# Performance work log

Measured on AMD Instinct MI355X. Metric: run time of the kernel, lower is better.

## Reference

```python
import jax, jax.numpy as jnp
import numpy as np

B, S, DIM = 2, 2048, 2048
H = 16
Q_LORA, KV_LORA = 1536, 512
D_NOPE, D_ROPE, D_V = 128, 64, 128
D_QK = D_NOPE + D_ROPE  # 192
SCALE = D_QK ** -0.5
EPS = 1e-6
NEG = -1e30


def rmsnorm(x, w):
    return x * jax.lax.rsqrt(jnp.mean(x * x, axis=-1, keepdims=True) + EPS) * w


def apply_rope(x, cos, sin):
    # x: [..., S, ..., d] with adjacent-pair complex layout (torch view_as_complex)
    d2 = x.shape[-1] // 2
    xr = x.reshape(x.shape[:-1] + (d2, 2))
    x0, x1 = xr[..., 0], xr[..., 1]
    bshape = (1, cos.shape[0]) + (1,) * (x.ndim - 3) + (d2,)
    c, s = cos.reshape(bshape), sin.reshape(bshape)
    o0 = x0 * c - x1 * s
    o1 = x0 * s + x1 * c
    return jnp.stack([o0, o1], axis=-1).reshape(x.shape)


def setup_inputs() -> dict:
    key = jax.random.key(0)
    ks = jax.random.split(key, 6)
    inv_freq = 1.0 / (10000.0 ** (np.arange(0, D_ROPE, 2, dtype=np.float32) / D_ROPE))
    ang = np.arange(S, dtype=np.float32)[:, None] * inv_freq[None, :]  # [S, 32]
    return {
        "x": jax.random.normal(ks[0], (B, S, DIM), jnp.float32),
        "wq_a": jax.random.normal(ks[1], (Q_LORA, DIM), jnp.float32) * (DIM ** -0.5),
        "q_norm_w": jnp.ones((Q_LORA,), jnp.float32),
        "wq_b": jax.random.normal(ks[2], (H * D_QK, Q_LORA), jnp.float32) * (Q_LORA ** -0.5),
        "wkv_a": jax.random.normal(ks[3], (KV_LORA + D_ROPE, DIM), jnp.float32) * (DIM ** -0.5),
        "kv_norm_w": jnp.ones((KV_LORA,), jnp.float32),
        "wkv_b": jax.random.normal(ks[4], (H * (D_NOPE + D_V), KV_LORA), jnp.float32) * (KV_LORA ** -0.5),
        "wo": jax.random.normal(ks[5], (DIM, H * D_V), jnp.float32) * ((H * D_V) ** -0.5),
        "cos": jnp.asarray(np.cos(ang)),
        "sin": jnp.asarray(np.sin(ang)),
    }


def reference(x, wq_a, q_norm_w, wq_b, wkv_a, kv_norm_w, wkv_b, wo, cos, sin):
    b, s, _ = x.shape
    # low-rank query projection: wq_b(q_norm(wq_a(x)))
    q = jnp.einsum('bsd,rd->bsr', x, wq_a)
    q = rmsnorm(q, q_norm_w)
    q = jnp.einsum('bsr,or->bso', q, wq_b).reshape(b, s, H, D_QK)
    q_nope, q_pe = q[..., :D_NOPE], q[..., D_NOPE:]
    q_pe = apply_rope(q_pe, cos, sin)  # [b,s,h,64]

    # joint kv latent + rope key
    kv = jnp.einsum('bsd,od->bso', x, wkv_a)
    kv_c, k_pe = kv[..., :KV_LORA], kv[..., KV_LORA:]
    k_pe = apply_rope(k_pe, cos, sin)          # [b,t,64]
    kv_c = rmsnorm(kv_c, kv_norm_w)            # [b,t,c] latent kv cache

    # absorbed wkv_b: [H, d_nope+d_v, c]
    wkv_b_r = wkv_b.reshape(H, D_NOPE + D_V, KV_LORA)
    w_nope, w_v = wkv_b_r[:, :D_NOPE, :], wkv_b_r[:, D_NOPE:, :]

    q_abs = jnp.einsum('bshd,hdc->bshc', q_nope, w_nope)  # absorb K up-proj into q
    scores = (jnp.einsum('bshc,btc->bsht', q_abs, kv_c) +
              jnp.einsum('bshr,btr->bsht', q_pe, k_pe)) * SCALE

    causal = jnp.tril(jnp.ones((s, s), bool))  # [s, t]
    scores = jnp.where(causal[:, None, :], scores, NEG)

    attn = jax.nn.softmax(scores.astype(jnp.float32), axis=-1).astype(x.dtype)
    o = jnp.einsum('bsht,btc->bshc', attn, kv_c)       # attend in latent space
    o = jnp.einsum('bshc,hdc->bshd', o, w_v)           # absorb V up-proj
    out = jnp.einsum('bsf,of->bso', o.reshape(b, s, H * D_V), wo)
    return out
```

## Files before the change

kernel.cpp:

```cpp
#include <hip/hip_runtime.h>
#include <hip/hip_bf16.h>
#include <stdint.h>

#define B_    2
#define S_    2048
#define DIM_  2048
#define H_    16
#define QL_   1536
#define KVL_  512
#define DN_   128
#define DR_   64
#define DV_   128
#define DQK_  192
#define NKV_  576
#define NKVP_ 640
#define BS_   (B_*S_)
#define SCALE_ 0.07216878364870322f

typedef __hip_bfloat16 bf16;
typedef float f32x4 __attribute__((ext_vector_type(4)));
typedef short bf16x8 __attribute__((ext_vector_type(8)));

#define BMT 128
#define BNT 128
#define BKT 64

__device__ __forceinline__ void gload_lds16(const void* g, void* l) {
#if __has_builtin(__builtin_amdgcn_global_load_lds)
  __builtin_amdgcn_global_load_lds(
      (const __attribute__((address_space(1))) void*)g,
      (__attribute__((address_space(3))) void*)l, 16, 0, 0);
#else
  *(uint4*)l = *(const uint4*)g;
#endif
}

template <int K, int LDA, int LDB, int LDC, int FLAGS>
__global__ __launch_bounds__(512, 4) void gemm_t(
    const bf16* __restrict__ A, long saz,
    const bf16* __restrict__ Bm, long sbz,
    void* __restrict__ Cv, long scz)
{
  int z = blockIdx.z;
  A  += (long)z * saz;
  Bm += (long)z * sbz;
  long coff = (long)z * scz;

  int gx = gridDim.x;
  int lin = blockIdx.y * gx + blockIdx.x;
  int nwg = gx * gridDim.y;
  int wg = (lin & 7) * (nwg >> 3) + (lin >> 3);
  int ry = wg / gx, col0 = (wg % gx) * BNT;

  int tid = threadIdx.x, lane = tid & 63, wave = tid >> 6;
  int wm = (wave >> 2) * 64, wn = (wave & 3) * 32;
  int quad = lane >> 4, l16 = lane & 15;

  __shared__ __align__(16) bf16 Asm[BMT * BKT];
  __shared__ __align__(16) bf16 Bsm[BNT * BKT];

  const int npass = (FLAGS & 16) ? 2 : 1;
  const int nty = gridDim.y * ((FLAGS & 16) ? 2 : 1);

  for (int p = 0; p < npass; ++p) {
    int rt = (p == 0) ? ry : (nty - 1 - ry);
    int row0 = rt * BMT;

    if (FLAGS & 2) { if (col0 > row0 + (BMT - 1)) continue; }
    int kend = K;
    if (FLAGS & 4) { int lim = row0 + BMT; if (lim < kend) kend = lim; }

    f32x4 acc[4][2] = {};

    for (int k0 = 0; k0 < kend; k0 += BKT) {
      __syncthreads();
#pragma unroll
      for (int t = 0; t < 2; ++t) {
        int c = (wave * 2 + t) * 64 + lane;
        int m = c >> 3, jx = c & 7, j = jx ^ (m & 7);
        gload_lds16(A  + (long)((row0 + m) * LDA + k0 + j * 8), Asm + c * 8);
        gload_lds16(Bm + (long)((col0 + m) * LDB + k0 + j * 8), Bsm + c * 8);
      }
      __syncthreads();
#pragma unroll
      for (int kk = 0; kk < BKT; kk += 32) {
        int jl = (kk >> 3) + quad;
        bf16x8 af[4], bfv[2];
#pragma unroll
        for (int i = 0; i < 4; ++i) {
          int m = wm + i * 16 + l16;
          af[i]  = *(const bf16x8*)(Asm + m * 64 + ((jl ^ (m & 7)) * 8));
        }
#pragma unroll
        for (int jn = 0; jn < 2; ++jn) {
          int n = wn + jn * 16 + l16;
          bfv[jn] = *(const bf16x8*)(Bsm + n * 64 + ((jl ^ (n & 7)) * 8));
        }
#pragma unroll
        for (int i = 0; i < 4; ++i)
#pragma unroll
          for (int jn = 0; jn < 2; ++jn)
            acc[i][jn] = __builtin_amdgcn_mfma_f32_16x16x32_bf16(af[i], bfv[jn], acc[i][jn], 0, 0, 0);
      }
    }

    if (FLAGS & 1) {
      float* C = (float*)Cv + coff;
#pragma unroll
      for (int i = 0; i < 4; ++i)
#pragma unroll
        for (int jn = 0; jn < 2; ++jn)
#pragma unroll
          for (int r = 0; r < 4; ++r) {
            int rr = row0 + wm + i * 16 + quad * 4 + r;
            int cc = col0 + wn + jn * 16 + l16;
            C[(long)rr * LDC + cc] = acc[i][jn][r];
          }
    } else if (FLAGS & 8) {
      bf16* C = (bf16*)Cv + coff;
#pragma unroll
      for (int i = 0; i < 4; ++i)
#pragma unroll
        for (int jn = 0; jn < 2; ++jn)
#pragma unroll
          for (int r = 0; r < 4; ++r) {
            int rr = row0 + wm + i * 16 + quad * 4 + r;
            int cc = col0 + wn + jn * 16 + l16;
            C[(long)rr * LDC + cc] = __float2bfloat16(acc[i][jn][r] * SCALE_);
          }
    } else {
      bf16* C = (bf16*)Cv + coff;
#pragma unroll
      for (int i = 0; i < 4; ++i)
#pragma unroll
        for (int jn = 0; jn < 2; ++jn)
#pragma unroll
          for (int r = 0; r < 4; ++r) {
            int rr = row0 + wm + i * 16 + quad * 4 + r;
            int cc = col0 + wn + jn * 16 + l16;
            C[(long)rr * LDC + cc] = __float2bfloat16(acc[i][jn][r]);
          }
    }
  }
}

template <int K, int LDA, int LDB, int LDC, int FLAGS>
static inline void G(hipStream_t st, const bf16* A, long saz, const bf16* Bp, long sbz,
                     void* C, long scz, int M, int N, int Z) {
  int gy = M / BMT;
  if (FLAGS & 16) gy >>= 1;
  dim3 g(N / BNT, gy, Z);
  gemm_t<K, LDA, LDB, LDC, FLAGS><<<g, 512, 0, st>>>(A, saz, Bp, sbz, C, scz);
}

__device__ __forceinline__ float wsum(float v) {
#pragma unroll
  for (int o = 32; o > 0; o >>= 1) v += __shfl_down(v, o, 64);
  return v;
}

#define CVT_N0  8388608L
#define CVT_N1 11534336L
#define CVT_N2 16252928L
#define CVT_N3 18350080L
#define CVT_N4 22544384L
#define CVT_N5 23855104L
__device__ __forceinline__ void cvt8(const float* __restrict__ s, bf16* __restrict__ d) {
  float4 a = ((const float4*)s)[0], b = ((const float4*)s)[1];
  __align__(16) bf16 t[8];
  t[0] = __float2bfloat16(a.x); t[1] = __float2bfloat16(a.y);
  t[2] = __float2bfloat16(a.z); t[3] = __float2bfloat16(a.w);
  t[4] = __float2bfloat16(b.x); t[5] = __float2bfloat16(b.y);
  t[6] = __float2bfloat16(b.z); t[7] = __float2bfloat16(b.w);
  *(uint4*)d = *(const uint4*)t;
}
__global__ __launch_bounds__(256) void cvt_all(
    const float* __restrict__ x, const float* __restrict__ wq_a,
    const float* __restrict__ wq_b, const float* __restrict__ wkv_b,
    const float* __restrict__ wo, const float* __restrict__ wkv_a,
    bf16* __restrict__ xb, bf16* __restrict__ wqab, bf16* __restrict__ wqbb,
    bf16* __restrict__ wkvbb, bf16* __restrict__ wob, bf16* __restrict__ wkvab)
{
  const long ngrp = CVT_N5 / 8;
  for (long v = (long)blockIdx.x * 256 + threadIdx.x; v < ngrp; v += (long)gridDim.x * 256) {
    long i = v * 8;
    if (i < CVT_N0) {
      cvt8(x + i, xb + i);
    } else if (i < CVT_N1) {
      long j = i - CVT_N0; cvt8(wq_a + j, wqab + j);
    } else if (i < CVT_N2) {
      long j = i - CVT_N1; cvt8(wq_b + j, wqbb + j);
    } else if (i < CVT_N3) {
      long j = i - CVT_N2; cvt8(wkv_b + j, wkvbb + j);
    } else if (i < CVT_N4) {
      long j = i - CVT_N3; cvt8(wo + j, wob + j);
    } else {
      long j = i - CVT_N4;
      if (j < (long)NKV_ * DIM_) cvt8(wkv_a + j, wkvab + j);
      else { __align__(16) bf16 t[8] = {}; *(uint4*)(wkvab + j) = *(const uint4*)t; }
    }
  }
}

__global__ __launch_bounds__(256) void rmsnorm_qa(bf16* __restrict__ qa, const float* __restrict__ w) {
  long row = blockIdx.x;
  bf16* pr = qa + row * QL_;
  int tid = threadIdx.x, lane = tid & 63, wave = tid >> 6;
  float v[6]; float ss = 0.f;
#pragma unroll
  for (int k = 0; k < 6; ++k) { int c = tid + k * 256; v[k] = __bfloat162float(pr[c]); ss += v[k] * v[k]; }
  ss = wsum(ss);
  __shared__ float sred[4];
  if (lane == 0) sred[wave] = ss;
  __syncthreads();
  float tot = sred[0] + sred[1] + sred[2] + sred[3];
  float scl = rsqrtf(tot / (float)QL_ + 1e-6f);
#pragma unroll
  for (int k = 0; k < 6; ++k) { int c = tid + k * 256; pr[c] = __float2bfloat16(v[k] * scl * w[c]); }
}

__global__ __launch_bounds__(256) void kv_post(const float* __restrict__ kvraw, const float* __restrict__ kvw,
                                               const float* __restrict__ cosb, const float* __restrict__ sinb,
                                               bf16* __restrict__ kfull) {
  int bs = blockIdx.x;
  int s = bs & (S_ - 1);
  const float* rowp = kvraw + (long)bs * NKVP_;
  bf16* outp = kfull + (long)bs * NKV_;
  int tid = threadIdx.x, lane = tid & 63, wave = tid >> 6;
  float v0 = rowp[tid], v1 = rowp[tid + 256];
  float ss = v0 * v0 + v1 * v1;
  ss = wsum(ss);
  __shared__ float sred[4];
  if (lane == 0) sred[wave] = ss;
  __syncthreads();
  float tot = sred[0] + sred[1] + sred[2] + sred[3];
  float scl = rsqrtf(tot / (float)KVL_ + 1e-6f);
  outp[tid]       = __float2bfloat16(v0 * scl * kvw[tid]);
  outp[tid + 256] = __float2bfloat16(v1 * scl * kvw[tid + 256]);
  if (tid < 32) {
    float x0 = rowp[KVL_ + 2 * tid], x1 = rowp[KVL_ + 2 * tid + 1];
    float c = cosb[s * 32 + tid], sn = sinb[s * 32 + tid];
    outp[KVL_ + 2 * tid]     = __float2bfloat16(x0 * c - x1 * sn);
    outp[KVL_ + 2 * tid + 1] = __float2bfloat16(x0 * sn + x1 * c);
  }
}

__global__ __launch_bounds__(256) void rope_q(bf16* __restrict__ qb,
                                              const float* __restrict__ cosb,
                                              const float* __restrict__ sinb) {
  int tx = threadIdx.x & 31, ty = threadIdx.x >> 5;
  long row = (long)blockIdx.x * 8 + ty;
  long bs = row >> 4; int h = (int)(row & 15); int s = (int)(bs & (S_ - 1));
  bf16* p = qb + bs * (H_ * DQK_) + h * DQK_ + DN_;
  float x0 = __bfloat162float(p[2 * tx]), x1 = __bfloat162float(p[2 * tx + 1]);
  float c = cosb[s * 32 + tx], sn = sinb[s * 32 + tx];
  p[2 * tx]     = __float2bfloat16(x0 * c - x1 * sn);
  p[2 * tx + 1] = __float2bfloat16(x0 * sn + x1 * c);
}

__global__ __launch_bounds__(256) void kpe_fill(const bf16* __restrict__ kfull, bf16* __restrict__ kvabs) {
  const long n = (long)B_ * H_ * S_ * 64;
  for (long i = (long)blockIdx.x * 256 + threadIdx.x; i < n; i += (long)gridDim.x * 256) {
    int d = (int)(i & 63);
    long t = (i >> 6) & (S_ - 1);
    int h = (int)((i >> 17) & 15);
    int b = (int)(i >> 21);
    kvabs[(((long)(b * H_ + h) * S_) + t) * DQK_ + DN_ + d] =
        kfull[((long)b * S_ + t) * NKV_ + KVL_ + d];
  }
}

__global__ __launch_bounds__(256) void transpose_kv(const bf16* __restrict__ kfull, bf16* __restrict__ kvT) {
  __shared__ bf16 tile[32][33];
  int b = blockIdx.z;
  int s0 = blockIdx.x * 32, c0 = blockIdx.y * 32;
  int tx = threadIdx.x & 31, ty = threadIdx.x >> 5;
#pragma unroll
  for (int r = 0; r < 4; ++r) {
    int s = s0 + ty + r * 8;
    tile[ty + r * 8][tx] = kfull[((long)b * S_ + s) * NKV_ + c0 + tx];
  }
  __syncthreads();
#pragma unroll
  for (int r = 0; r < 4; ++r) {
    int c = c0 + ty + r * 8;
    kvT[(long)b * KVL_ * S_ + (long)c * S_ + s0 + tx] = tile[tx][ty + r * 8];
  }
}

__global__ __launch_bounds__(256) void softmax_causal(bf16* __restrict__ sc) {
  int wave = threadIdx.x >> 6, lane = threadIdx.x & 63;
  int r = blockIdx.x * 4 + wave, z = blockIdx.y;
  bf16* row = sc + ((long)z * S_ + r) * S_;
  int wlen = (r & ~127) + 128;
  int base0 = lane * 8;

  float v[4][8];
  float mx = -3.0e38f;
#pragma unroll
  for (int c = 0; c < 4; ++c) {
    int cb = c * 512;
    if (cb <= r) {
      int base = cb + base0;
      __align__(16) bf16 t8[8];
      *(bf16x8*)t8 = *(const bf16x8*)(row + base);
      if (cb + 511 <= r) {
#pragma unroll
        for (int j = 0; j < 8; ++j) {
          float f = __bfloat162float(t8[j]);
          v[c][j] = f; mx = fmaxf(mx, f);
        }
      } else {
#pragma unroll
        for (int j = 0; j < 8; ++j) {
          float f = (base + j <= r) ? __bfloat162float(t8[j]) : -3.0e38f;
          v[c][j] = f; mx = fmaxf(mx, f);
        }
      }
    }
  }
#pragma unroll
  for (int o = 32; o > 0; o >>= 1) mx = fmaxf(mx, __shfl_xor(mx, o, 64));

  float s = 0.f;
#pragma unroll
  for (int c = 0; c < 4; ++c) {
    if (c * 512 <= r) {
#pragma unroll
      for (int j = 0; j < 8; ++j) {
        float e = __expf(v[c][j] - mx);
        v[c][j] = e; s += e;
      }
    }
  }
#pragma unroll
  for (int o = 32; o > 0; o >>= 1) s += __shfl_xor(s, o, 64);
  float inv = 1.f / s;

#pragma unroll
  for (int c = 0; c < 4; ++c) {
    int base = c * 512 + base0;
    if (c * 512 <= r && base < wlen) {
      __align__(16) bf16 t8[8];
#pragma unroll
      for (int j = 0; j < 8; ++j) t8[j] = __float2bfloat16(v[c][j] * inv);
      *(bf16x8*)(row + base) = *(const bf16x8*)t8;
    }
  }
}

template <int HC>
static void attn_loop(hipStream_t stream, const bf16* qb, const bf16* kvabs,
                      const bf16* kvT, const bf16* wkvbb,
                      bf16* ovb, bf16* scores_c, bf16* ob_c) {
  const int nch = B_ * (H_ / HC);
  for (int ch = 0; ch < nch; ++ch) {
    int b = ch / (H_ / HC), hq = ch % (H_ / HC), h0 = hq * HC;

    G<DQK_, H_ * DQK_, DQK_, S_, 8 | 2>(stream,
        qb + (long)b * S_ * (H_ * DQK_) + (long)h0 * DQK_, DQK_,
        kvabs + (long)(b * H_ + h0) * S_ * DQK_, (long)S_ * DQK_,
        scores_c, (long)S_ * S_, S_, S_, HC);
    softmax_causal<<<dim3(S_ / 4, HC), 256, 0, stream>>>(scores_c);
    G<S_, S_, S_, HC * KVL_, 4 | 16>(stream,
        scores_c, (long)S_ * S_, kvT + (long)b * KVL_ * S_, 0,
        ob_c, KVL_, S_, KVL_, HC);
    G<KVL_, HC * KVL_, KVL_, H_ * DV_, 0>(stream,
        ob_c, KVL_, wkvbb + ((long)h0 * 256 + DN_) * KVL_, (long)256 * KVL_,
        ovb + (long)b * S_ * (H_ * DV_) + (long)h0 * DV_, DV_, S_, DV_, HC);
  }
}

extern "C" void kernel_launch(void* const* d_in, const int* in_sizes, int n_in,
                              void* d_out, int out_size, void* d_ws, size_t ws_size,
                              hipStream_t stream) {
  const float* x     = (const float*)d_in[0];
  const float* wq_a  = (const float*)d_in[1];
  const float* qnw   = (const float*)d_in[2];
  const float* wq_b  = (const float*)d_in[3];
  const float* wkv_a = (const float*)d_in[4];
  const float* kvnw  = (const float*)d_in[5];
  const float* wkv_b = (const float*)d_in[6];
  const float* wo    = (const float*)d_in[7];
  const float* cosb  = (const float*)d_in[8];
  const float* sinb  = (const float*)d_in[9];
  float* out = (float*)d_out;
  (void)in_sizes; (void)n_in; (void)out_size;

  int hc;
  if      (ws_size >= 256376832UL) hc = 16;
  else if (ws_size >= 172490752UL) hc = 8;
  else                             hc = 4;

  char* base = (char*)d_ws;
  long off = 0;
  auto at = [&](long bytes) { char* r = base + off; off += bytes; return r; };

  bf16* qb    = (bf16*)at(25165824L);
  bf16* ovb   = (bf16*)at(16777216L);
  bf16* kfull = (bf16*)at(4718592L);
  bf16* kvT   = (bf16*)at(4194304L);
  bf16* wkvbb = (bf16*)at(4194304L);
  bf16* wob   = (bf16*)at(8388608L);
  bf16* kvabs = (bf16*)at(25165824L);
  char* ov = base + off;

  bf16*  xb    = (bf16*) (ov);
  bf16*  wqab  = (bf16*) (ov + 16777216L);
  bf16*  wqbb  = (bf16*) (ov + 23068672L);
  bf16*  qa    = (bf16*) (ov + 32505856L);
  float* kvraw = (float*)qa;

  bf16* scores_c = (bf16*)ov;
  bf16* ob_c     = (bf16*)(ov + (long)hc * 8388608L);

  bf16* wkvab = kvT;

  cvt_all<<<4096, 256, 0, stream>>>(x, wq_a, wq_b, wkv_b, wo, wkv_a,
                                    xb, wqab, wqbb, wkvbb, wob, wkvab);

  G<DIM_, DIM_, DIM_, QL_, 0>(stream, xb, 0, wqab, 0, qa, 0, BS_, QL_, 1);
  rmsnorm_qa<<<BS_, 256, 0, stream>>>(qa, qnw);
  G<QL_, QL_, QL_, H_ * DQK_, 0>(stream, qa, 0, wqbb, 0, qb, 0, BS_, H_ * DQK_, 1);
  rope_q<<<BS_ * H_ / 8, 256, 0, stream>>>(qb, cosb, sinb);

  G<DIM_, DIM_, DIM_, NKVP_, 1>(stream, xb, 0, wkvab, 0, kvraw, 0, BS_, NKVP_, 1);
  kv_post<<<BS_, 256, 0, stream>>>(kvraw, kvnw, cosb, sinb, kfull);
  transpose_kv<<<dim3(S_ / 32, KVL_ / 32, B_), 256, 0, stream>>>(kfull, kvT);

  for (int b = 0; b < B_; ++b)
    G<KVL_, NKV_, KVL_, DQK_, 0>(stream,
        kfull + (long)b * S_ * NKV_, 0, wkvbb, (long)256 * KVL_,
        kvabs + (long)b * H_ * S_ * DQK_, (long)S_ * DQK_, S_, DN_, H_);
  kpe_fill<<<8192, 256, 0, stream>>>(kfull, kvabs);

  if (hc == 16)
    attn_loop<16>(stream, qb, kvabs, kvT, wkvbb, ovb, scores_c, ob_c);
  else if (hc == 8)
    attn_loop<8>(stream, qb, kvabs, kvT, wkvbb, ovb, scores_c, ob_c);
  else
    attn_loop<4>(stream, qb, kvabs, kvT, wkvbb, ovb, scores_c, ob_c);

  G<H_ * DV_, H_ * DV_, H_ * DV_, DIM_, 1>(stream, ovb, 0, wob, 0, out, 0, BS_, DIM_, 1);
}
```

Measured before the change: 588.9 us.

## Pre-absorb V up-projection into latent KV to shrink attention PV GEMM

Computes a per-batch V matrix (kv_c times w_v for all heads), stored transposed, once before the attention loop. The PV GEMM then contracts directly to the 128-wide head output instead of the 512-wide latent, and the separate w_v GEMM, transpose kernel and intermediate buffer are dropped. This cuts the dominant causal PV FLOPs roughly fourfold. The cost is an extra absorb GEMM with a strided transposed-store epilogue and a larger workspace buffer.

```diff
diff --git a/kernel.cpp b/kernel.cpp
--- a/kernel.cpp
+++ b/kernel.cpp
@@ -52,6 +52,10 @@
   int wg = (lin & 7) * (nwg >> 3) + (lin >> 3);
   int ry = wg / gx, col0 = (wg % gx) * BNT;
 
+  const long bbase = (FLAGS & 32)
+      ? (((long)(col0 >> 7) * 256 + 128) * (long)LDB)
+      : ((long)col0 * (long)LDB);
+
   int tid = threadIdx.x, lane = tid & 63, wave = tid >> 6;
   int wm = (wave >> 2) * 64, wn = (wave & 3) * 32;
   int quad = lane >> 4, l16 = lane & 15;
@@ -79,7 +83,7 @@
         int c = (wave * 2 + t) * 64 + lane;
         int m = c >> 3, jx = c & 7, j = jx ^ (m & 7);
         gload_lds16(A  + (long)((row0 + m) * LDA + k0 + j * 8), Asm + c * 8);
-        gload_lds16(Bm + (long)((col0 + m) * LDB + k0 + j * 8), Bsm + c * 8);
+        gload_lds16(Bm + bbase + (long)m * LDB + k0 + j * 8, Bsm + c * 8);
       }
       __syncthreads();
 #pragma unroll
@@ -128,6 +132,19 @@
             int cc = col0 + wn + jn * 16 + l16;
             C[(long)rr * LDC + cc] = __float2bfloat16(acc[i][jn][r] * SCALE_);
           }
+    } else if (FLAGS & 64) {
+      bf16* C = (bf16*)Cv + coff;
+#pragma unroll
+      for (int i = 0; i < 4; ++i)
+#pragma unroll
+        for (int jn = 0; jn < 2; ++jn) {
+          int rr = row0 + wm + i * 16 + quad * 4;
+          int cc = col0 + wn + jn * 16 + l16;
+          __align__(8) bf16 t4[4];
+#pragma unroll
+          for (int r = 0; r < 4; ++r) t4[r] = __float2bfloat16(acc[i][jn][r]);
+          *(short4*)(C + (long)cc * LDC + rr) = *(const short4*)t4;
+        }
     } else {
       bf16* C = (bf16*)Cv + coff;
 #pragma unroll
@@ -270,24 +287,6 @@
   }
 }
 
-__global__ __launch_bounds__(256) void transpose_kv(const bf16* __restrict__ kfull, bf16* __restrict__ kvT) {
-  __shared__ bf16 tile[32][33];
-  int b = blockIdx.z;
-  int s0 = blockIdx.x * 32, c0 = blockIdx.y * 32;
-  int tx = threadIdx.x & 31, ty = threadIdx.x >> 5;
-#pragma unroll
-  for (int r = 0; r < 4; ++r) {
-    int s = s0 + ty + r * 8;
-    tile[ty + r * 8][tx] = kfull[((long)b * S_ + s) * NKV_ + c0 + tx];
-  }
-  __syncthreads();
-#pragma unroll
-  for (int r = 0; r < 4; ++r) {
-    int c = c0 + ty + r * 8;
-    kvT[(long)b * KVL_ * S_ + (long)c * S_ + s0 + tx] = tile[tx][ty + r * 8];
-  }
-}
-
 __global__ __launch_bounds__(256) void softmax_causal(bf16* __restrict__ sc) {
   int wave = threadIdx.x >> 6, lane = threadIdx.x & 63;
   int r = blockIdx.x * 4 + wave, z = blockIdx.y;
@@ -351,8 +350,8 @@
 
 template <int HC>
 static void attn_loop(hipStream_t stream, const bf16* qb, const bf16* kvabs,
-                      const bf16* kvT, const bf16* wkvbb,
-                      bf16* ovb, bf16* scores_c, bf16* ob_c) {
+                      const bf16* VabsT,
+                      bf16* ovb, bf16* scores_c) {
   const int nch = B_ * (H_ / HC);
   for (int ch = 0; ch < nch; ++ch) {
     int b = ch / (H_ / HC), hq = ch % (H_ / HC), h0 = hq * HC;
@@ -362,11 +361,9 @@
         kvabs + (long)(b * H_ + h0) * S_ * DQK_, (long)S_ * DQK_,
         scores_c, (long)S_ * S_, S_, S_, HC);
     softmax_causal<<<dim3(S_ / 4, HC), 256, 0, stream>>>(scores_c);
-    G<S_, S_, S_, HC * KVL_, 4 | 16>(stream,
-        scores_c, (long)S_ * S_, kvT + (long)b * KVL_ * S_, 0,
-        ob_c, KVL_, S_, KVL_, HC);
-    G<KVL_, HC * KVL_, KVL_, H_ * DV_, 0>(stream,
-        ob_c, KVL_, wkvbb + ((long)h0 * 256 + DN_) * KVL_, (long)256 * KVL_,
+    G<S_, S_, S_, H_ * DV_, 4 | 16>(stream,
+        scores_c, (long)S_ * S_,
+        VabsT + (long)b * S_ * S_ + (long)h0 * DV_ * S_, (long)DV_ * S_,
         ovb + (long)b * S_ * (H_ * DV_) + (long)h0 * DV_, DV_, S_, DV_, HC);
   }
 }
@@ -388,8 +385,8 @@
   (void)in_sizes; (void)n_in; (void)out_size;
 
   int hc;
-  if      (ws_size >= 256376832UL) hc = 16;
-  else if (ws_size >= 172490752UL) hc = 8;
+  if      (ws_size >= 235405312UL) hc = 16;
+  else if (ws_size >= 168296448UL) hc = 8;
   else                             hc = 4;
 
   char* base = (char*)d_ws;
@@ -399,10 +396,10 @@
   bf16* qb    = (bf16*)at(25165824L);
   bf16* ovb   = (bf16*)at(16777216L);
   bf16* kfull = (bf16*)at(4718592L);
-  bf16* kvT   = (bf16*)at(4194304L);
   bf16* wkvbb = (bf16*)at(4194304L);
   bf16* wob   = (bf16*)at(8388608L);
   bf16* kvabs = (bf16*)at(25165824L);
+  bf16* VabsT = (bf16*)at(16777216L);
   char* ov = base + off;
 
   bf16*  xb    = (bf16*) (ov);
@@ -412,9 +409,8 @@
   float* kvraw = (float*)qa;
 
   bf16* scores_c = (bf16*)ov;
-  bf16* ob_c     = (bf16*)(ov + (long)hc * 8388608L);
-
-  bf16* wkvab = kvT;
+
+  bf16* wkvab = VabsT;
 
   cvt_all<<<4096, 256, 0, stream>>>(x, wq_a, wq_b, wkv_b, wo, wkv_a,
                                     xb, wqab, wqbb, wkvbb, wob, wkvab);
@@ -426,7 +422,6 @@
 
   G<DIM_, DIM_, DIM_, NKVP_, 1>(stream, xb, 0, wkvab, 0, kvraw, 0, BS_, NKVP_, 1);
   kv_post<<<BS_, 256, 0, stream>>>(kvraw, kvnw, cosb, sinb, kfull);
-  transpose_kv<<<dim3(S_ / 32, KVL_ / 32, B_), 256, 0, stream>>>(kfull, kvT);
 
   for (int b = 0; b < B_; ++b)
     G<KVL_, NKV_, KVL_, DQK_, 0>(stream,
@@ -434,12 +429,16 @@
         kvabs + (long)b * H_ * S_ * DQK_, (long)S_ * DQK_, S_, DN_, H_);
   kpe_fill<<<8192, 256, 0, stream>>>(kfull, kvabs);
 
+  G<KVL_, NKV_, KVL_, S_, 32 | 64>(stream,
+      kfull, (long)S_ * NKV_, wkvbb, 0,
+      VabsT, (long)S_ * S_, S_, H_ * DV_, B_);
+
   if (hc == 16)
-    attn_loop<16>(stream, qb, kvabs, kvT, wkvbb, ovb, scores_c, ob_c);
+    attn_loop<16>(stream, qb, kvabs, VabsT, ovb, scores_c);
   else if (hc == 8)
-    attn_loop<8>(stream, qb, kvabs, kvT, wkvbb, ovb, scores_c, ob_c);
+    attn_loop<8>(stream, qb, kvabs, VabsT, ovb, scores_c);
   else
-    attn_loop<4>(stream, qb, kvabs, kvT, wkvbb, ovb, scores_c, ob_c);
+    attn_loop<4>(stream, qb, kvabs, VabsT, ovb, scores_c);
 
   G<H_ * DV_, H_ * DV_, H_ * DV_, DIM_, 1>(stream, ovb, 0, wob, 0, out, 0, BS_, DIM_, 1);
 }
```

Result: faster. 543.5 us (-7.7%).
